# Kernel optimization log

Hardware: AMD Instinct MI355X
Metric: run time of the kernel (lower is better)

Reference implementation:

```python
import jax, jax.numpy as jnp
import numpy as np

N = 65536          # particles
E = 524288         # relations (avg degree 8)
RIG = 4096         # rigid instance = particles [0, RIG); fluid = [RIG, N)
PSTEPS = 2
ATTR, STATE, RELD, NF = 3, 6, 1, 128
DT = 1.0 / 60.0
MEAN_P = np.zeros(3, np.float32); STD_P = np.ones(3, np.float32)
MEAN_V = np.zeros(3, np.float32); STD_V = np.ones(3, np.float32)


def _lin(x, w, b):
    return x @ w.T + b  # torch Linear convention: w is [out, in]


def setup_inputs() -> dict:
    key = jax.random.key(0)
    ks = iter(jax.random.split(key, 40))
    d = {}
    d["state"] = jax.random.normal(next(ks), (N, STATE), jnp.float32)
    d["attr"] = jax.random.normal(next(ks), (N, ATTR), jnp.float32)
    d["Ra"] = jax.random.normal(next(ks), (E, RELD), jnp.float32)
    d["rel_recv"] = jax.random.randint(next(ks), (E,), 0, N, jnp.int32)
    d["rel_send"] = jax.random.randint(next(ks), (E,), 0, N, jnp.int32)

    def w(shape):
        return jax.random.normal(next(ks), shape, jnp.float32) / np.sqrt(shape[1])

    d["pe_w0"] = w((NF, ATTR + 2 * STATE)); d["pe_b0"] = jnp.zeros(NF)
    d["pe_w1"] = w((NF, NF)); d["pe_b1"] = jnp.zeros(NF)
    d["re_w0"] = w((NF, 2 * ATTR + 4 * STATE + RELD)); d["re_b0"] = jnp.zeros(NF)
    d["re_w1"] = w((NF, NF)); d["re_b1"] = jnp.zeros(NF)
    d["re_w2"] = w((NF, NF)); d["re_b2"] = jnp.zeros(NF)
    d["rp_w"] = w((NF, 3 * NF)); d["rp_b"] = jnp.zeros(NF)
    d["pp_w"] = w((NF, 2 * NF)); d["pp_b"] = jnp.zeros(NF)
    d["rg_w0"] = w((NF, NF)); d["rg_b0"] = jnp.zeros(NF)
    d["rg_w1"] = w((NF, NF)); d["rg_b1"] = jnp.zeros(NF)
    d["rg_w2"] = w((7, NF)); d["rg_b2"] = jnp.zeros(7)
    d["fl_w0"] = w((NF, NF)); d["fl_b0"] = jnp.zeros(NF)
    d["fl_w1"] = w((NF, NF)); d["fl_b1"] = jnp.zeros(NF)
    d["fl_w2"] = w((3, NF)); d["fl_b2"] = jnp.zeros(3)
    return d


def reference(state, attr, Ra, rel_recv, rel_send,
              pe_w0, pe_b0, pe_w1, pe_b1,
              re_w0, re_b0, re_w1, re_b1, re_w2, re_b2,
              rp_w, rp_b, pp_w, pp_b,
              rg_w0, rg_b0, rg_w1, rg_b1, rg_w2, rg_b2,
              fl_w0, fl_b0, fl_w1, fl_b1, fl_w2, fl_b2):
    relu = jax.nn.relu
    mean_p = jnp.asarray(MEAN_P); std_p = jnp.asarray(STD_P)
    mean_v = jnp.asarray(MEAN_V); std_v = jnp.asarray(STD_V)

    # rigid-body offset (state minus instance centroid for the rigid instance)
    offset = jnp.zeros_like(state).at[:RIG].set(
        state[:RIG] - jnp.mean(state[:RIG], axis=0))
    attr2 = jnp.concatenate([attr, offset], axis=1)        # [N, ATTR+STATE]

    # f_O^enc: particle encoder on [attr2, state]
    pe_in = jnp.concatenate([attr2, state], axis=1)         # [N, 15]
    particle_encode = relu(_lin(relu(_lin(pe_in, pe_w0, pe_b0)), pe_w1, pe_b1))

    # f_R^enc: relation encoder on gathered receiver/sender features
    rel_in = jnp.concatenate([attr2[rel_recv], attr2[rel_send],
                              state[rel_recv], state[rel_send], Ra], axis=1)  # [E, 31]
    h = relu(_lin(rel_in, re_w0, re_b0))
    h = relu(_lin(h, re_w1, re_b1))
    relation_encode = relu(_lin(h, re_w2, re_b2))           # [E, NF]

    # propagation: gather effects -> f_R -> scatter-add -> f_O
    effect = jnp.zeros((N, NF), state.dtype)
    for _ in range(PSTEPS):
        r_eff = effect[rel_recv]                            # [E, NF]
        s_eff = effect[rel_send]                            # [E, NF]
        rel_eff = relu(_lin(jnp.concatenate(
            [relation_encode, r_eff, s_eff], axis=1), rp_w, rp_b))
        agg = jax.ops.segment_sum(rel_eff, rel_recv, num_segments=N)  # Rr @ rel_eff
        effect = relu(_lin(jnp.concatenate(
            [particle_encode, agg], axis=1), pp_w, pp_b))   # residual=False

    # rigid predictor: quaternion + translation of the rigid body
    pooled = jnp.mean(effect[:RIG], axis=0)                 # [NF]
    t = _lin(relu(_lin(relu(_lin(pooled, rg_w0, rg_b0)), rg_w1, rg_b1)), rg_w2, rg_b2)
    q = t[:4] / jnp.linalg.norm(t[:4])
    w, x, y, z = q[0], q[1], q[2], q[3]
    R = jnp.stack([
        jnp.stack([1.0 - 2 * (y * y + z * z), 2 * (x * y + z * w), 2 * (x * z - y * w)]),
        jnp.stack([2 * (x * y - z * w), 1.0 - 2 * (x * x + z * z), 2 * (y * z + x * w)]),
        jnp.stack([2 * (x * z + y * w), 2 * (y * z - x * w), 1.0 - 2 * (x * x + y * y)]),
    ])
    b = t[4:] * std_p
    p0 = state[:RIG, :3] * std_p + mean_p
    c = jnp.mean(p0, axis=0)
    p1 = (p0 - c) @ R + b + c
    v = (p1 - p0) / DT
    pred_rigid = (v - mean_v) / std_v                       # [RIG, 3]

    # fluid predictor: per-particle MLP
    f = relu(_lin(effect[RIG:], fl_w0, fl_b0))
    f = relu(_lin(f, fl_w1, fl_b1))
    pred_fluid = _lin(f, fl_w2, fl_b2)                      # [N-RIG, 3]

    return jnp.concatenate([pred_rigid, pred_fluid], axis=0)  # [N, 3]
```

## Files before the change

kernel.cpp:

```cpp
#include <hip/hip_runtime.h>
#include <hip/hip_bf16.h>
#include <cstdio>

#define N_P   65536
#define N_E   524288
#define RIG_  4096

typedef __attribute__((ext_vector_type(8))) short bf16x8;
typedef __attribute__((ext_vector_type(4))) float f32x4;
typedef unsigned short u16;
typedef unsigned int   u32;

__device__ __forceinline__ u16 f2b(float x) {
    __hip_bfloat16 h = __float2bfloat16(x);
    return *(u16*)&h;
}
__device__ __forceinline__ float b2f(u16 u) {
    union { unsigned u; float f; } c; c.u = ((unsigned)u) << 16; return c.f;
}
__device__ __forceinline__ unsigned pk2(float x, float y) {
    return (unsigned)f2b(x) | ((unsigned)f2b(y) << 16);
}
#define MFMA(a,b,c) __builtin_amdgcn_mfma_f32_16x16x32_bf16((a),(b),(c),0,0,0)

__device__ __forceinline__ void bar_l() {
    asm volatile("s_waitcnt lgkmcnt(0)\n\ts_barrier" ::: "memory");
}

__global__ __launch_bounds__(256) void k_hist(const int* __restrict__ recv,
                                              u32* __restrict__ cnt) {
    int i = blockIdx.x * 256 + threadIdx.x;
    if (i < N_E) atomicAdd(&cnt[recv[i]], 1u);
}
__global__ __launch_bounds__(256) void k_scan1(u32* __restrict__ data,
                                               u32* __restrict__ bsum) {
    __shared__ u32 s[256];
    int t = threadIdx.x, g = blockIdx.x * 256 + t;
    u32 v = data[g];
    s[t] = v; __syncthreads();
    for (int o = 1; o < 256; o <<= 1) {
        u32 x = (t >= o) ? s[t - o] : 0u;
        __syncthreads(); s[t] += x; __syncthreads();
    }
    data[g] = s[t] - v;
    if (t == 255) bsum[blockIdx.x] = s[255];
}
__global__ __launch_bounds__(256) void k_scan2(u32* __restrict__ bsum) {
    __shared__ u32 s[256];
    int t = threadIdx.x;
    u32 v = bsum[t];
    s[t] = v; __syncthreads();
    for (int o = 1; o < 256; o <<= 1) {
        u32 x = (t >= o) ? s[t - o] : 0u;
        __syncthreads(); s[t] += x; __syncthreads();
    }
    bsum[t] = s[t] - v;
}
__global__ __launch_bounds__(256) void k_scan3(u32* __restrict__ data,
                                               const u32* __restrict__ bsum) {
    int g = blockIdx.x * 256 + threadIdx.x;
    data[g] += bsum[blockIdx.x];
}
__global__ __launch_bounds__(256) void k_scatter(const int* __restrict__ recv,
                                                 const int* __restrict__ send,
                                                 u32* __restrict__ head,
                                                 int4* __restrict__ edges) {
    int i = blockIdx.x * 256 + threadIdx.x;
    if (i < N_E) {
        int n = recv[i];
        u32 pos = atomicAdd(&head[n], 1u);
        edges[pos] = make_int4(n, send[i], i, 0);
    }
}

struct CvtJob { const float* src; u16* dst; int n; int mode; int bstart; };
struct CvtArgs { CvtJob j[14]; };

__global__ __launch_bounds__(256) void k_cvt_all(CvtArgs a) {
    int b = blockIdx.x;
    int ji = 0;
    #pragma unroll
    for (int k = 1; k < 14; k++) if (b >= a.j[k].bstart) ji = k;
    CvtJob jb = a.j[ji];
    int i = (b - jb.bstart) * 256 + threadIdx.x;
    if (i >= jb.n) return;
    if (jb.mode == 0) {
        jb.dst[i] = f2b(jb.src[i]);
    } else if (jb.mode == 2) {
        int r = i >> 7;
        jb.dst[i] = (r < 3) ? f2b(jb.src[i]) : 0;
    } else if (jb.mode == 3) {
        int r = i >> 7, c = i & 127;
        jb.dst[i] = f2b(jb.src[r * 384 + c]);
    } else if (jb.mode == 4) {
        int r = i >> 7, c = i & 127;
        jb.dst[i] = f2b(jb.src[r * 256 + c]);
    } else if (jb.mode == 5) {
        int r = i >> 5, c = i & 31;
        float v = 0.f;
        if (c < 9)       v = jb.src[r * 31 + c];
        else if (c < 15) v = jb.src[r * 31 + 18 + (c - 9)];
        jb.dst[i] = f2b(v);
    } else if (jb.mode == 6) {
        int r = i >> 5, c = i & 31;
        float v = 0.f;
        if (c < 9)       v = jb.src[r * 31 + 9 + c];
        else if (c < 15) v = jb.src[r * 31 + 24 + (c - 9)];
        jb.dst[i] = f2b(v);
    } else {
        int r = i >> 5, c = i & 31;
        jb.dst[i] = (c < 15) ? f2b(jb.src[r * 15 + c]) : 0;
    }
}

__global__ __launch_bounds__(256) void k_centroid(const float* __restrict__ state,
                                                  float* __restrict__ cent) {
    int d = blockIdx.x;
    __shared__ float red[256];
    float s = 0.f;
    for (int r = threadIdx.x; r < RIG_; r += 256) s += state[r * 6 + d];
    red[threadIdx.x] = s; __syncthreads();
    for (int o = 128; o > 0; o >>= 1) {
        if (threadIdx.x < o) red[threadIdx.x] += red[threadIdx.x + o];
        __syncthreads();
    }
    if (threadIdx.x == 0) cent[d] = red[0] / (float)RIG_;
}

__global__ __launch_bounds__(256) void k_particle_ext(
        const float* __restrict__ state, const float* __restrict__ attr,
        const float* __restrict__ cent,
        const u16* __restrict__ w0r, const u16* __restrict__ w0s,
        const u16* __restrict__ pew0, const float* __restrict__ pe_b0,
        const u16* __restrict__ pew1, const float* __restrict__ pe_b1,
        const u16* __restrict__ wp,
        u16* __restrict__ P, u16* __restrict__ Q, u16* __restrict__ T) {
    __shared__ float in_s[64][16];
    __shared__ u16 INF[64 * 32];
    __shared__ __align__(16) u16 BUF[64 * 128];
    __shared__ float b0_s[128], b1_s[128];
    int t = threadIdx.x;
    int base = blockIdx.x * 64;
    if (t < 128) { b0_s[t] = pe_b0[t]; b1_s[t] = pe_b1[t]; }
    for (int it = t; it < 64 * 15; it += 256) {
        int r = it / 15, c = it % 15;
        int p = base + r;
        float v;
        if (c < 3)      v = attr[p * 3 + c];
        else if (c < 9) v = (p < RIG_) ? (state[p * 6 + (c - 3)] - cent[c - 3]) : 0.0f;
        else            v = state[p * 6 + (c - 9)];
        in_s[r][c] = v;
    }
    __syncthreads();
    int wv = t >> 6, kq4 = (t >> 4) & 3, m = t & 15;
    {
        int e = wv * 16 + m;
        u16 tmp[8];
        #pragma unroll
        for (int j = 0; j < 8; j++) {
            int k = kq4 * 8 + j;
            tmp[j] = (k < 15) ? f2b(in_s[e][k]) : (u16)0;
        }
        *(uint4*)&INF[((wv * 4 + kq4) * 16 + m) * 8] = *(uint4*)tmp;
    }
    int lane = t & 63, mm = lane & 15, quad = lane >> 4;
    bf16x8 af0 = *(const bf16x8*)&INF[((wv * 4 + quad) * 16 + mm) * 8];
    {
        f32x4 acc[8] = {};
        #pragma unroll
        for (int nt = 0; nt < 8; nt++) {
            bf16x8 bf = *(const bf16x8*)(w0r + (size_t)(nt * 16 + mm) * 32 + quad * 8);
            acc[nt] = MFMA(af0, bf, acc[nt]);
        }
        #pragma unroll
        for (int nt = 0; nt < 8; nt++) {
            int col = nt * 16 + mm;
            #pragma unroll
            for (int rg = 0; rg < 4; rg++) {
                int row = wv * 16 + quad * 4 + rg;
                P[(size_t)(base + row) * 128 + col] = f2b(acc[nt][rg]);
            }
        }
    }
    {
        f32x4 acc[8] = {};
        #pragma unroll
        for (int nt = 0; nt < 8; nt++) {
            bf16x8 bf = *(const bf16x8*)(w0s + (size_t)(nt * 16 + mm) * 32 + quad * 8);
            acc[nt] = MFMA(af0, bf, acc[nt]);
        }
        #pragma unroll
        for (int nt = 0; nt < 8; nt++) {
            int col = nt * 16 + mm;
            #pragma unroll
            for (int rg = 0; rg < 4; rg++) {
                int row = wv * 16 + quad * 4 + rg;
                Q[(size_t)(base + row) * 128 + col] = f2b(acc[nt][rg]);
            }
        }
    }
    {
        f32x4 acc[8] = {};
        #pragma unroll
        for (int nt = 0; nt < 8; nt++) {
            bf16x8 bf = *(const bf16x8*)(pew0 + (size_t)(nt * 16 + mm) * 32 + quad * 8);
            acc[nt] = MFMA(af0, bf, acc[nt]);
        }
        #pragma unroll
        for (int nt = 0; nt < 8; nt++) {
            int col = nt * 16 + mm;
            #pragma unroll
            for (int rg = 0; rg < 4; rg++) {
                BUF[((wv * 16 + (col >> 3)) * 16 + quad * 4 + rg) * 8 + (col & 7)] =
                    f2b(fmaxf(acc[nt][rg] + b0_s[col], 0.f));
            }
        }
    }
    {
        f32x4 acc[8] = {};
        for (int kc = 0; kc < 4; kc++) {
            bf16x8 af = *(const bf16x8*)&BUF[((wv * 16 + kc * 4 + quad) * 16 + mm) * 8];
            #pragma unroll
            for (int nt = 0; nt < 8; nt++) {
                bf16x8 bf = *(const bf16x8*)(pew1 + (size_t)(nt * 16 + mm) * 128 + kc * 32 + quad * 8);
                acc[nt] = MFMA(af, bf, acc[nt]);
            }
        }
        #pragma unroll
        for (int nt = 0; nt < 8; nt++) {
            int col = nt * 16 + mm;
            #pragma unroll
            for (int rg = 0; rg < 4; rg++) {
                BUF[((wv * 16 + (col >> 3)) * 16 + quad * 4 + rg) * 8 + (col & 7)] =
                    f2b(fmaxf(acc[nt][rg] + b1_s[col], 0.f));
            }
        }
    }
    {
        f32x4 acc[8] = {};
        for (int kc = 0; kc < 4; kc++) {
            bf16x8 af = *(const bf16x8*)&BUF[((wv * 16 + kc * 4 + quad) * 16 + mm) * 8];
            #pragma unroll
            for (int nt = 0; nt < 8; nt++) {
                bf16x8 bf = *(const bf16x8*)(wp + (size_t)(nt * 16 + mm) * 128 + kc * 32 + quad * 8);
                acc[nt] = MFMA(af, bf, acc[nt]);
            }
        }
        #pragma unroll
        for (int nt = 0; nt < 8; nt++) {
            int col = nt * 16 + mm;
            #pragma unroll
            for (int rg = 0; rg < 4; rg++) {
                int row = wv * 16 + quad * 4 + rg;
                T[(size_t)(base + row) * 128 + col] = f2b(acc[nt][rg]);
            }
        }
    }
}

__global__ __launch_bounds__(512, 4) void k_rel(
        const u16* __restrict__ P, const u16* __restrict__ Q,
        const float* __restrict__ Ra, const int4* __restrict__ edges,
        const float* __restrict__ re_w0_raw, const float* __restrict__ b0,
        const u16* __restrict__ w1b, const float* __restrict__ b1,
        const u16* __restrict__ w2b, const float* __restrict__ b2,
        const u16* __restrict__ wreb, const float* __restrict__ rpb,
        u16* __restrict__ Z, float* __restrict__ agg) {
    __shared__ __align__(16) u16 BUFA[64 * 136];
    __shared__ __align__(16) u16 BUFB[64 * 136];
    __shared__ int rv_s[2][64];
    __shared__ float wRa_s[128], b0_s[128], rpb_s[128];
    int t = threadIdx.x;
    if (t < 128) {
        wRa_s[t] = re_w0_raw[t * 31 + 30];
        b0_s[t] = b0[t]; rpb_s[t] = rpb[t];
    }
    int w = t >> 6, lane = t & 63, mm = lane & 15, quad = lane >> 4;
    int colw = w * 16 + mm;
    bf16x8 W1f[4], W2f[4], WEf[4];
    #pragma unroll
    for (int kc = 0; kc < 4; kc++) {
        W1f[kc] = *(const bf16x8*)(w1b  + (size_t)colw * 128 + kc * 32 + quad * 8);
        W2f[kc] = *(const bf16x8*)(w2b  + (size_t)colw * 128 + kc * 32 + quad * 8);
        WEf[kc] = *(const bf16x8*)(wreb + (size_t)colw * 128 + kc * 32 + quad * 8);
    }
    float b1c = b1[colw], b2c = b2[colw];
    int es = t >> 3, cs2 = (t & 7) * 2;
    int egs = es >> 4, ms = es & 15;
    int sseg = t >> 7, cseg = t & 127;
    int zrow = t >> 3, zc0 = (t & 7) * 16;
    const long NT = N_E / 64;
    const long stride = gridDim.x;

    long tile = blockIdx.x;
    uint4 upC0, upC1, uqC0, uqC1; float raC; int rvC;
    {
        long nb = tile * 64;
        int4 e = edges[nb + es];
        rvC = edges[nb + (t & 63)].x;
        raC = Ra[e.z];
        upC0 = *(const uint4*)(P + (size_t)e.x * 128 + (size_t)cs2 * 8);
        upC1 = *(const uint4*)(P + (size_t)e.x * 128 + (size_t)(cs2 + 1) * 8);
        uqC0 = *(const uint4*)(Q + (size_t)e.y * 128 + (size_t)cs2 * 8);
        uqC1 = *(const uint4*)(Q + (size_t)e.y * 128 + (size_t)(cs2 + 1) * 8);
    }
    __syncthreads();
    int p = 0;
    for (; tile < NT; tile += stride) {
        long base = tile * 64;
        long ntile = tile + stride;
        bool hn = ntile < NT;
        int4 eN = make_int4(0, 0, 0, 0); int rvN = 0;
        if (hn) {
            long nb = ntile * 64;
            eN  = edges[nb + es];
            rvN = edges[nb + (t & 63)].x;
        }
        if (t < 64) rv_s[p][t] = rvC;
        {
            #pragma unroll
            for (int ci = 0; ci < 2; ci++) {
                int kq = cs2 + ci;
                uint4 up = ci ? upC1 : upC0;
                uint4 uq = ci ? uqC1 : uqC0;
                const u16* pp = (const u16*)&up; const u16* qq = (const u16*)&uq;
                u16 outv[8];
                #pragma unroll
                for (int j = 0; j < 8; j++) {
                    int c = kq * 8 + j;
                    float v = b2f(pp[j]) + b2f(qq[j]) + raC * wRa_s[c] + b0_s[c];
                    outv[j] = f2b(fmaxf(v, 0.f));
                }
                *(uint4*)&BUFA[((egs * 16 + kq) * 16 + ms) * 8] = *(uint4*)outv;
            }
        }
        bar_l();
        uint4 upN0{}, upN1{}, uqN0{}, uqN1{}; float raN = 0.f;
        if (hn) {
            raN  = Ra[eN.z];
            upN0 = *(const uint4*)(P + (size_t)eN.x * 128 + (size_t)cs2 * 8);
            upN1 = *(const uint4*)(P + (size_t)eN.x * 128 + (size_t)(cs2 + 1) * 8);
            uqN0 = *(const uint4*)(Q + (size_t)eN.y * 128 + (size_t)cs2 * 8);
            uqN1 = *(const uint4*)(Q + (size_t)eN.y * 128 + (size_t)(cs2 + 1) * 8);
        }
        {
            f32x4 acc[4] = {};
            #pragma unroll
            for (int eg = 0; eg < 4; eg++)
                #pragma unroll
                for (int kc = 0; kc < 4; kc++) {
                    bf16x8 af = *(const bf16x8*)&BUFA[((eg * 16 + kc * 4 + quad) * 16 + mm) * 8];
                    acc[eg] = MFMA(af, W1f[kc], acc[eg]);
                }
            #pragma unroll
            for (int eg = 0; eg < 4; eg++)
                #pragma unroll
                for (int rg = 0; rg < 4; rg++)
                    BUFB[((eg * 16 + (colw >> 3)) * 16 + quad * 4 + rg) * 8 + (colw & 7)] =
                        f2b(fmaxf(acc[eg][rg] + b1c, 0.f));
        }
        bar_l();
        {
            f32x4 acc[4] = {};
            #pragma unroll
            for (int eg = 0; eg < 4; eg++)
                #pragma unroll
                for (int kc = 0; kc < 4; kc++) {
                    bf16x8 af = *(const bf16x8*)&BUFB[((eg * 16 + kc * 4 + quad) * 16 + mm) * 8];
                    acc[eg] = MFMA(af, W2f[kc], acc[eg]);
                }
            #pragma unroll
            for (int eg = 0; eg < 4; eg++)
                #pragma unroll
                for (int rg = 0; rg < 4; rg++)
                    BUFA[((eg * 16 + (colw >> 3)) * 16 + quad * 4 + rg) * 8 + (colw & 7)] =
                        f2b(fmaxf(acc[eg][rg] + b2c, 0.f));
        }
        bar_l();
        {
            f32x4 zacc[4] = {};
            #pragma unroll
            for (int eg = 0; eg < 4; eg++)
                #pragma unroll
                for (int kc = 0; kc < 4; kc++) {
                    bf16x8 af = *(const bf16x8*)&BUFA[((eg * 16 + kc * 4 + quad) * 16 + mm) * 8];
                    zacc[eg] = MFMA(af, WEf[kc], zacc[eg]);
                }
            #pragma unroll
            for (int eg = 0; eg < 4; eg++)
                #pragma unroll
                for (int rg = 0; rg < 4; rg++)
                    BUFB[(eg * 16 + quad * 4 + rg) * 136 + colw] = f2b(zacc[eg][rg]);
        }
        bar_l();
        {
            uint4 z0 = *(const uint4*)&BUFB[zrow * 136 + zc0];
            uint4 z1 = *(const uint4*)&BUFB[zrow * 136 + zc0 + 8];
            *(uint4*)&Z[(base + zrow) * 128 + zc0]     = z0;
            *(uint4*)&Z[(base + zrow) * 128 + zc0 + 8] = z1;
        }
        {
            int r0 = sseg * 16;
            int cur = rv_s[p][r0];
            float a = fmaxf(b2f(BUFB[r0 * 136 + cseg]) + rpb_s[cseg], 0.f);
            bool first = true;
            for (int rr = r0 + 1; rr < r0 + 16; rr++) {
                int n = rv_s[p][rr];
                float v = fmaxf(b2f(BUFB[rr * 136 + cseg]) + rpb_s[cseg], 0.f);
                if (n == cur) a += v;
                else {
                    if (first) atomicAdd(&agg[(size_t)cur * 128 + cseg], a);
                    else       agg[(size_t)cur * 128 + cseg] = a;
                    first = false; cur = n; a = v;
                }
            }
            atomicAdd(&agg[(size_t)cur * 128 + cseg], a);
        }
        if (hn) { upC0 = upN0; upC1 = upN1; uqC0 = uqN0; uqC1 = uqN1; raC = raN; rvC = rvN; }
        p ^= 1;
    }
}

__global__ __launch_bounds__(256) void k_node2(
        const float* __restrict__ agg, const u16* __restrict__ T,
        const u16* __restrict__ wab, const float* __restrict__ ppb,
        const u16* __restrict__ wrb, const u16* __restrict__ wsb,
        u16* __restrict__ U, u16* __restrict__ V) {
    __shared__ __align__(16) u16 AF[64 * 128];
    int t = threadIdx.x;
    long base = (long)blockIdx.x * 64;
    int wv = t >> 6, kq4 = (t >> 4) & 3, m = t & 15;
    {
        long node = base + wv * 16 + m;
        #pragma unroll
        for (int i = 0; i < 4; i++) {
            int kq = kq4 + 4 * i;
            const float* src = agg + node * 128 + kq * 8;
            float4 f0 = *(const float4*)src, f1 = *(const float4*)(src + 4);
            uint4 v;
            v.x = pk2(f0.x, f0.y); v.y = pk2(f0.z, f0.w);
            v.z = pk2(f1.x, f1.y); v.w = pk2(f1.z, f1.w);
            *(uint4*)&AF[((wv * 16 + kq) * 16 + m) * 8] = v;
        }
    }
    int lane = t & 63, mm = lane & 15, quad = lane >> 4;
    f32x4 acc[8] = {};
    for (int kc = 0; kc < 4; kc++) {
        bf16x8 af = *(const bf16x8*)&AF[((wv * 16 + kc * 4 + quad) * 16 + mm) * 8];
        #pragma unroll
        for (int nt = 0; nt < 8; nt++) {
            bf16x8 bf = *(const bf16x8*)(wab + (size_t)(nt * 16 + mm) * 128 + kc * 32 + quad * 8);
            acc[nt] = MFMA(af, bf, acc[nt]);
        }
    }
    #pragma unroll
    for (int nt = 0; nt < 8; nt++) {
        int col = nt * 16 + mm;
        #pragma unroll
        for (int rg = 0; rg < 4; rg++) {
            long row = base + wv * 16 + quad * 4 + rg;
            float v = acc[nt][rg] + b2f(T[row * 128 + col]) + ppb[col];
            u16 e = f2b(fmaxf(v, 0.f));
            AF[((wv * 16 + (col >> 3)) * 16 + quad * 4 + rg) * 8 + (col & 7)] = e;
        }
    }
    {
        f32x4 au[8] = {};
        for (int kc = 0; kc < 4; kc++) {
            bf16x8 af = *(const bf16x8*)&AF[((wv * 16 + kc * 4 + quad) * 16 + mm) * 8];
            #pragma unroll
            for (int nt = 0; nt < 8; nt++) {
                bf16x8 bu = *(const bf16x8*)(wrb + (size_t)(nt * 16 + mm) * 128 + kc * 32 + quad * 8);
                au[nt] = MFMA(af, bu, au[nt]);
            }
        }
        #pragma unroll
        for (int nt = 0; nt < 8; nt++) {
            int col = nt * 16 + mm;
            #pragma unroll
            for (int rg = 0; rg < 4; rg++) {
                long row = base + wv * 16 + quad * 4 + rg;
                U[row * 128 + col] = f2b(au[nt][rg]);
            }
        }
    }
    {
        f32x4 av[8] = {};
        for (int kc = 0; kc < 4; kc++) {
            bf16x8 af = *(const bf16x8*)&AF[((wv * 16 + kc * 4 + quad) * 16 + mm) * 8];
            #pragma unroll
            for (int nt = 0; nt < 8; nt++) {
                bf16x8 bv = *(const bf16x8*)(wsb + (size_t)(nt * 16 + mm) * 128 + kc * 32 + quad * 8);
                av[nt] = MFMA(af, bv, av[nt]);
            }
        }
        #pragma unroll
        for (int nt = 0; nt < 8; nt++) {
            int col = nt * 16 + mm;
            #pragma unroll
            for (int rg = 0; rg < 4; rg++) {
                long row = base + wv * 16 + quad * 4 + rg;
                V[row * 128 + col] = f2b(av[nt][rg]);
            }
        }
    }
}

#define HPAD 136
__global__ __launch_bounds__(256) void k_node2fl(
        const float* __restrict__ agg, const u16* __restrict__ T,
        const u16* __restrict__ wab, const float* __restrict__ ppb,
        float* __restrict__ pooledsum,
        const u16* __restrict__ w0b, const float* __restrict__ b0,
        const u16* __restrict__ w1b, const float* __restrict__ b1,
        const u16* __restrict__ w2b, const float* __restrict__ b2,
        float* __restrict__ out) {
    __shared__ __align__(16) u16 H[64 * HPAD];
    int t = threadIdx.x;
    long base = (long)blockIdx.x * 64;
    bool fluid = (base >= RIG_);
    int wv = t >> 6, kq4 = (t >> 4) & 3, m = t & 15;
    {
        long node = base + wv * 16 + m;
        #pragma unroll
        for (int i = 0; i < 4; i++) {
            int kq = kq4 + 4 * i;
            const float* src = agg + node * 128 + kq * 8;
            float4 f0 = *(const float4*)src, f1 = *(const float4*)(src + 4);
            uint4 v;
            v.x = pk2(f0.x, f0.y); v.y = pk2(f0.z, f0.w);
            v.z = pk2(f1.x, f1.y); v.w = pk2(f1.z, f1.w);
            *(uint4*)&H[((wv * 16 + kq) * 16 + m) * 8] = v;
        }
    }
    int lane = t & 63, mm = lane & 15, quad = lane >> 4;
    f32x4 acc[8] = {};
    for (int kc = 0; kc < 4; kc++) {
        bf16x8 af = *(const bf16x8*)&H[((wv * 16 + kc * 4 + quad) * 16 + mm) * 8];
        #pragma unroll
        for (int nt = 0; nt < 8; nt++) {
            bf16x8 bf = *(const bf16x8*)(wab + (size_t)(nt * 16 + mm) * 128 + kc * 32 + quad * 8);
            acc[nt] = MFMA(af, bf, acc[nt]);
        }
    }
    __syncthreads();
    #pragma unroll
    for (int nt = 0; nt < 8; nt++) {
        int col = nt * 16 + mm;
        #pragma unroll
        for (int rg = 0; rg < 4; rg++) {
            long row = base + wv * 16 + quad * 4 + rg;
            float v = acc[nt][rg] + b2f(T[row * 128 + col]) + ppb[col];
            H[(wv * 16 + quad * 4 + rg) * HPAD + col] = f2b(fmaxf(v, 0.f));
        }
    }
    if (!fluid) {
        bar_l();
        int col = t & 127, half = t >> 7;
        float s = 0.f;
        for (int r = half * 32; r < half * 32 + 32; r++)
            s += b2f(H[r * HPAD + col]);
        atomicAdd(&pooledsum[col], s);
        return;
    }
    {
        f32x4 a8[8] = {};
        for (int kc = 0; kc < 4; kc++) {
            bf16x8 af = *(const bf16x8*)&H[(wv * 16 + mm) * HPAD + kc * 32 + quad * 8];
            #pragma unroll
            for (int nt = 0; nt < 8; nt++) {
                bf16x8 bf = *(const bf16x8*)(w0b + (size_t)(nt * 16 + mm) * 128 + kc * 32 + quad * 8);
                a8[nt] = MFMA(af, bf, a8[nt]);
            }
        }
        #pragma unroll
        for (int nt = 0; nt < 8; nt++) {
            int col = nt * 16 + mm;
            float bv = b0[col];
            #pragma unroll
            for (int rg = 0; rg < 4; rg++) {
                int row = wv * 16 + quad * 4 + rg;
                H[row * HPAD + col] = f2b(fmaxf(a8[nt][rg] + bv, 0.f));
            }
        }
    }
    {
        f32x4 a8[8] = {};
        for (int kc = 0; kc < 4; kc++) {
            bf16x8 af = *(const bf16x8*)&H[(wv * 16 + mm) * HPAD + kc * 32 + quad * 8];
            #pragma unroll
            for (int nt = 0; nt < 8; nt++) {
                bf16x8 bf = *(const bf16x8*)(w1b + (size_t)(nt * 16 + mm) * 128 + kc * 32 + quad * 8);
                a8[nt] = MFMA(af, bf, a8[nt]);
            }
        }
        #pragma unroll
        for (int nt = 0; nt < 8; nt++) {
            int col = nt * 16 + mm;
            float bv = b1[col];
            #pragma unroll
            for (int rg = 0; rg < 4; rg++) {
                int row = wv * 16 + quad * 4 + rg;
                H[row * HPAD + col] = f2b(fmaxf(a8[nt][rg] + bv, 0.f));
            }
        }
    }
    {
        f32x4 a1 = {};
        for (int kc = 0; kc < 4; kc++) {
            bf16x8 af = *(const bf16x8*)&H[(wv * 16 + mm) * HPAD + kc * 32 + quad * 8];
            bf16x8 bf = *(const bf16x8*)(w2b + (size_t)mm * 128 + kc * 32 + quad * 8);
            a1 = MFMA(af, bf, a1);
        }
        if (mm < 3) {
            float bv = b2[mm];
            #pragma unroll
            for (int rg = 0; rg < 4; rg++) {
                long row = base + wv * 16 + quad * 4 + rg;
                out[row * 3 + mm] = a1[rg] + bv;
            }
        }
    }
}

__global__ __launch_bounds__(256) void k_edge2(
        const u16* __restrict__ Z, const u16* __restrict__ U, const u16* __restrict__ V,
        const int4* __restrict__ edges,
        const float* __restrict__ rpb, float* __restrict__ agg) {
    __shared__ __align__(16) u16 S16[64 * 136];
    __shared__ int rv_s[64];
    __shared__ float rpb_s[128];
    int t = threadIdx.x;
    long base = (long)blockIdx.x * 64;
    if (t < 64) rv_s[t] = edges[base + t].x;
    if (t < 128) rpb_s[t] = rpb[t];
    int r = t >> 2, q = t & 3;
    int4 er = edges[base + r];
    long zb = (base + r) * 128;
    size_t ub = (size_t)er.x * 128, vb = (size_t)er.y * 128;
    bar_l();
    #pragma unroll
    for (int i = 0; i < 4; i++) {
        int c0 = q * 32 + i * 8;
        uint4 uz = *(const uint4*)(Z + zb + c0);
        uint4 uu = *(const uint4*)(U + ub + c0);
        uint4 uv = *(const uint4*)(V + vb + c0);
        const u16* zz = (const u16*)&uz; const u16* pu = (const u16*)&uu; const u16* pv = (const u16*)&uv;
        u16 o[8];
        #pragma unroll
        for (int j = 0; j < 8; j++)
            o[j] = f2b(fmaxf(b2f(zz[j]) + b2f(pu[j]) + b2f(pv[j]) + rpb_s[c0 + j], 0.f));
        *(uint4*)&S16[r * 136 + c0] = *(uint4*)o;
    }
    bar_l();
    {
        int s = t >> 7, col = t & 127;
        int r0 = s * 32;
        int cur = rv_s[r0];
        float a = b2f(S16[r0 * 136 + col]);
        bool first = true;
        for (int rr = r0 + 1; rr < r0 + 32; rr++) {
            int n = rv_s[rr];
            float v = b2f(S16[rr * 136 + col]);
            if (n == cur) a += v;
            else {
                if (first) atomicAdd(&agg[(size_t)cur * 128 + col], a);
                else       agg[(size_t)cur * 128 + col] = a;
                first = false; cur = n; a = v;
            }
        }
        atomicAdd(&agg[(size_t)cur * 128 + col], a);
    }
}

__global__ __launch_bounds__(128) void k_rigid_head(
        const float* __restrict__ pooledsum,
        const float* __restrict__ w0, const float* __restrict__ b0,
        const float* __restrict__ w1, const float* __restrict__ b1,
        const float* __restrict__ w2, const float* __restrict__ b2,
        float* __restrict__ rig) {
    __shared__ float pl[128], ha[128], hb[128], tv[7];
    int t = threadIdx.x;
    pl[t] = pooledsum[t] * (1.0f / (float)RIG_);
    __syncthreads();
    float a = b0[t];
    for (int k = 0; k < 128; k++) a += w0[t * 128 + k] * pl[k];
    ha[t] = fmaxf(a, 0.f);
    __syncthreads();
    a = b1[t];
    for (int k = 0; k < 128; k++) a += w1[t * 128 + k] * ha[k];
    hb[t] = fmaxf(a, 0.f);
    __syncthreads();
    if (t < 7) {
        float s = b2[t];
        for (int k = 0; k < 128; k++) s += w2[t * 128 + k] * hb[k];
        tv[t] = s;
    }
    __syncthreads();
    if (t == 0) {
        float w = tv[0], x = tv[1], y = tv[2], z = tv[3];
        float n = sqrtf(w * w + x * x + y * y + z * z);
        w /= n; x /= n; y /= n; z /= n;
        rig[0] = 1.f - 2.f * (y * y + z * z); rig[1] = 2.f * (x * y + z * w); rig[2] = 2.f * (x * z - y * w);
        rig[3] = 2.f * (x * y - z * w); rig[4] = 1.f - 2.f * (x * x + z * z); rig[5] = 2.f * (y * z + x * w);
        rig[6] = 2.f * (x * z + y * w); rig[7] = 2.f * (y * z - x * w); rig[8] = 1.f - 2.f * (x * x + y * y);
        rig[9] = tv[4]; rig[10] = tv[5]; rig[11] = tv[6];
    }
}

__global__ __launch_bounds__(256) void k_rigid_out(
        const float* __restrict__ state, const float* __restrict__ cent,
        const float* __restrict__ rig, float* __restrict__ out) {
    int i = blockIdx.x * 256 + threadIdx.x;
    if (i >= RIG_) return;
    float p0[3], d[3];
    #pragma unroll
    for (int k = 0; k < 3; k++) { p0[k] = state[i * 6 + k]; d[k] = p0[k] - cent[k]; }
    #pragma unroll
    for (int j = 0; j < 3; j++) {
        float p1 = rig[0 * 3 + j] * d[0] + rig[1 * 3 + j] * d[1] + rig[2 * 3 + j] * d[2]
                 + rig[9 + j] + cent[j];
        out[i * 3 + j] = (p1 - p0[j]) * 60.0f;
    }
}

extern "C" void kernel_launch(void* const* d_in, const int* in_sizes, int n_in,
                              void* d_out, int out_size, void* d_ws, size_t ws_size,
                              hipStream_t stream) {
    const float* state = (const float*)d_in[0];
    const float* attr  = (const float*)d_in[1];
    const float* Ra    = (const float*)d_in[2];
    const int*   recv  = (const int*)d_in[3];
    const int*   send  = (const int*)d_in[4];
    const float* pe_w0 = (const float*)d_in[5];  const float* pe_b0 = (const float*)d_in[6];
    const float* pe_w1 = (const float*)d_in[7];  const float* pe_b1 = (const float*)d_in[8];
    const float* re_w0 = (const float*)d_in[9];  const float* re_b0 = (const float*)d_in[10];
    const float* re_w1 = (const float*)d_in[11]; const float* re_b1 = (const float*)d_in[12];
    const float* re_w2 = (const float*)d_in[13]; const float* re_b2 = (const float*)d_in[14];
    const float* rp_w  = (const float*)d_in[15]; const float* rp_b  = (const float*)d_in[16];
    const float* pp_w  = (const float*)d_in[17]; const float* pp_b  = (const float*)d_in[18];
    const float* rg_w0 = (const float*)d_in[19]; const float* rg_b0 = (const float*)d_in[20];
    const float* rg_w1 = (const float*)d_in[21]; const float* rg_b1 = (const float*)d_in[22];
    const float* rg_w2 = (const float*)d_in[23]; const float* rg_b2 = (const float*)d_in[24];
    const float* fl_w0 = (const float*)d_in[25]; const float* fl_b0 = (const float*)d_in[26];
    const float* fl_w1 = (const float*)d_in[27]; const float* fl_b1 = (const float*)d_in[28];
    const float* fl_w2 = (const float*)d_in[29]; const float* fl_b2 = (const float*)d_in[30];
    float* out = (float*)d_out;

    char* p = (char*)d_ws;
    auto alloc = [&](size_t bytes) { char* r = p; p += (bytes + 255) / 256 * 256; return r; };
    float* cent    = (float*)alloc(8 * 4);
    float* pooled  = (float*)alloc(128 * 4);
    float* rig     = (float*)alloc(16 * 4);
    u32*   rowhead = (u32*)alloc((size_t)N_P * 4);
    u32*   bsum    = (u32*)alloc(256 * 4);
    int4*  edges   = (int4*)alloc((size_t)N_E * 16);
    float* agg     = (float*)alloc((size_t)N_P * 128 * 4);
    u16*   Z       = (u16*)alloc((size_t)N_E * 128 * 2);
    u16*   T       = (u16*)alloc((size_t)N_P * 128 * 2);
    u16*   P       = (u16*)alloc((size_t)N_P * 128 * 2);
    u16*   Q       = (u16*)alloc((size_t)N_P * 128 * 2);
    u16*   wreb    = (u16*)alloc(128 * 128 * 2);
    u16*   wrb     = (u16*)alloc(128 * 128 * 2);
    u16*   wsb     = (u16*)alloc(128 * 128 * 2);
    u16*   wpb     = (u16*)alloc(128 * 128 * 2);
    u16*   wab     = (u16*)alloc(128 * 128 * 2);
    u16*   rw1b    = (u16*)alloc(128 * 128 * 2);
    u16*   rw2b    = (u16*)alloc(128 * 128 * 2);
    u16*   pew1b   = (u16*)alloc(128 * 128 * 2);
    u16*   flw0b   = (u16*)alloc(128 * 128 * 2);
    u16*   flw1b   = (u16*)alloc(128 * 128 * 2);
    u16*   flw2b   = (u16*)alloc(16 * 128 * 2);
    u16*   w0rb    = (u16*)alloc(128 * 32 * 2);
    u16*   w0sb    = (u16*)alloc(128 * 32 * 2);
    u16*   pew0b   = (u16*)alloc(128 * 32 * 2);
    size_t need = (size_t)(p - (char*)d_ws);
    if (ws_size < need) {
        fprintf(stderr, "kernel_launch: ws_size %zu < needed %zu\n", ws_size, need);
        return;
    }
    u16* U = P; u16* V = Q;

    hipMemsetAsync(rowhead, 0, (size_t)N_P * 4, stream);
    k_hist<<<N_E / 256, 256, 0, stream>>>(recv, rowhead);
    k_scan1<<<N_P / 256, 256, 0, stream>>>(rowhead, bsum);
    k_scan2<<<1, 256, 0, stream>>>(bsum);
    k_scan3<<<N_P / 256, 256, 0, stream>>>(rowhead, bsum);
    k_scatter<<<N_E / 256, 256, 0, stream>>>(recv, send, rowhead, edges);

    CvtArgs ca;
    int bs = 0;
    auto addjob = [&](int idx, const float* s, u16* d, int n, int mode) {
        ca.j[idx] = {s, d, n, mode, bs};
        bs += (n + 255) / 256;
    };
    addjob(0,  rp_w,        wreb,  128 * 128, 3);
    addjob(1,  rp_w + 128,  wrb,   128 * 128, 3);
    addjob(2,  rp_w + 256,  wsb,   128 * 128, 3);
    addjob(3,  pp_w,        wpb,   128 * 128, 4);
    addjob(4,  pp_w + 128,  wab,   128 * 128, 4);
    addjob(5,  re_w1,       rw1b,  128 * 128, 0);
    addjob(6,  re_w2,       rw2b,  128 * 128, 0);
    addjob(7,  pe_w1,       pew1b, 128 * 128, 0);
    addjob(8,  fl_w0,       flw0b, 128 * 128, 0);
    addjob(9,  fl_w1,       flw1b, 128 * 128, 0);
    addjob(10, fl_w2,       flw2b, 16 * 128,  2);
    addjob(11, re_w0,       w0rb,  128 * 32,  5);
    addjob(12, re_w0,       w0sb,  128 * 32,  6);
    addjob(13, pe_w0,       pew0b, 128 * 32,  7);
    k_cvt_all<<<bs, 256, 0, stream>>>(ca);

    k_centroid<<<6, 256, 0, stream>>>(state, cent);
    k_particle_ext<<<N_P / 64, 256, 0, stream>>>(state, attr, cent,
                                                 w0rb, w0sb, pew0b, pe_b0,
                                                 pew1b, pe_b1, wpb, P, Q, T);

    hipMemsetAsync(agg, 0, (size_t)N_P * 128 * 4, stream);
    k_rel<<<512, 512, 0, stream>>>(P, Q, Ra, edges,
                                   re_w0, re_b0, rw1b, re_b1, rw2b, re_b2,
                                   wreb, rp_b, Z, agg);
    k_node2<<<N_P / 64, 256, 0, stream>>>(agg, T, wab, pp_b, wrb, wsb, U, V);

    hipMemsetAsync(agg, 0, (size_t)N_P * 128 * 4, stream);
    hipMemsetAsync(pooled, 0, 128 * 4, stream);
    k_edge2<<<N_E / 64, 256, 0, stream>>>(Z, U, V, edges, rp_b, agg);
    k_node2fl<<<N_P / 64, 256, 0, stream>>>(agg, T, wab, pp_b, pooled,
                                            flw0b, fl_b0, flw1b, fl_b1,
                                            flw2b, fl_b2, out);

    k_rigid_head<<<1, 128, 0, stream>>>(pooled, rg_w0, rg_b0, rg_w1, rg_b1, rg_w2, rg_b2, rig);
    k_rigid_out<<<(RIG_ + 255) / 256, 256, 0, stream>>>(state, cent, rig, out);
}
```

Before: 537.7 us.

## Retile k_rel MLP waves to 2x2 MFMA blocks and drop gather prefetch

Each wave now computes a 32-edge by 32-column tile (2x2 MFMA blocks) instead of 64 edges by 16 columns, so each LDS A-fragment load feeds two MFMAs. Register-resident W1/W2 fragments double per wave, and the third-layer weights are now reloaded from global memory every tile instead of being kept in registers. The software prefetch of the next tile's P/Q gathers is removed; gathers now happen synchronously at the start of each tile. The aim is to cut LDS traffic and register pressure, at the cost of exposing gather latency and adding repeated weight loads.

New measurement: 592.7 us. +10.2%, slower.

```diff
diff --git a/kernel.cpp b/kernel.cpp
--- a/kernel.cpp
+++ b/kernel.cpp
@@ -276,15 +276,22 @@
         b0_s[t] = b0[t]; rpb_s[t] = rpb[t];
     }
     int w = t >> 6, lane = t & 63, mm = lane & 15, quad = lane >> 4;
-    int colw = w * 16 + mm;
-    bf16x8 W1f[4], W2f[4], WEf[4];
+    int eh = w & 1, cq = w >> 1;
+    int e0 = eh * 2;
+    bf16x8 W1f[2][4], W2f[2][4];
+    float b1c[2], b2c[2];
+    int colc[2];
     #pragma unroll
-    for (int kc = 0; kc < 4; kc++) {
-        W1f[kc] = *(const bf16x8*)(w1b  + (size_t)colw * 128 + kc * 32 + quad * 8);
-        W2f[kc] = *(const bf16x8*)(w2b  + (size_t)colw * 128 + kc * 32 + quad * 8);
-        WEf[kc] = *(const bf16x8*)(wreb + (size_t)colw * 128 + kc * 32 + quad * 8);
-    }
-    float b1c = b1[colw], b2c = b2[colw];
+    for (int nt = 0; nt < 2; nt++) {
+        int col = cq * 32 + nt * 16 + mm;
+        colc[nt] = col;
+        #pragma unroll
+        for (int kc = 0; kc < 4; kc++) {
+            W1f[nt][kc] = *(const bf16x8*)(w1b + (size_t)col * 128 + kc * 32 + quad * 8);
+            W2f[nt][kc] = *(const bf16x8*)(w2b + (size_t)col * 128 + kc * 32 + quad * 8);
+        }
+        b1c[nt] = b1[col]; b2c[nt] = b2[col];
+    }
     int es = t >> 3, cs2 = (t & 7) * 2;
     int egs = es >> 4, ms = es & 15;
     int sseg = t >> 7, cseg = t & 127;
@@ -293,16 +300,11 @@
     const long stride = gridDim.x;
 
     long tile = blockIdx.x;
-    uint4 upC0, upC1, uqC0, uqC1; float raC; int rvC;
+    int4 eC; int rvC;
     {
         long nb = tile * 64;
-        int4 e = edges[nb + es];
+        eC = edges[nb + es];
         rvC = edges[nb + (t & 63)].x;
-        raC = Ra[e.z];
-        upC0 = *(const uint4*)(P + (size_t)e.x * 128 + (size_t)cs2 * 8);
-        upC1 = *(const uint4*)(P + (size_t)e.x * 128 + (size_t)(cs2 + 1) * 8);
-        uqC0 = *(const uint4*)(Q + (size_t)e.y * 128 + (size_t)cs2 * 8);
-        uqC1 = *(const uint4*)(Q + (size_t)e.y * 128 + (size_t)(cs2 + 1) * 8);
     }
     __syncthreads();
     int p = 0;
@@ -318,79 +320,92 @@
         }
         if (t < 64) rv_s[p][t] = rvC;
         {
+            float ra = Ra[eC.z];
             #pragma unroll
             for (int ci = 0; ci < 2; ci++) {
                 int kq = cs2 + ci;
-                uint4 up = ci ? upC1 : upC0;
-                uint4 uq = ci ? uqC1 : uqC0;
+                uint4 up = *(const uint4*)(P + (size_t)eC.x * 128 + (size_t)kq * 8);
+                uint4 uq = *(const uint4*)(Q + (size_t)eC.y * 128 + (size_t)kq * 8);
                 const u16* pp = (const u16*)&up; const u16* qq = (const u16*)&uq;
                 u16 outv[8];
                 #pragma unroll
                 for (int j = 0; j < 8; j++) {
                     int c = kq * 8 + j;
-                    float v = b2f(pp[j]) + b2f(qq[j]) + raC * wRa_s[c] + b0_s[c];
+                    float v = b2f(pp[j]) + b2f(qq[j]) + ra * wRa_s[c] + b0_s[c];
                     outv[j] = f2b(fmaxf(v, 0.f));
                 }
                 *(uint4*)&BUFA[((egs * 16 + kq) * 16 + ms) * 8] = *(uint4*)outv;
             }
         }
         bar_l();
-        uint4 upN0{}, upN1{}, uqN0{}, uqN1{}; float raN = 0.f;
-        if (hn) {
-            raN  = Ra[eN.z];
-            upN0 = *(const uint4*)(P + (size_t)eN.x * 128 + (size_t)cs2 * 8);
-            upN1 = *(const uint4*)(P + (size_t)eN.x * 128 + (size_t)(cs2 + 1) * 8);
-            uqN0 = *(const uint4*)(Q + (size_t)eN.y * 128 + (size_t)cs2 * 8);
-            uqN1 = *(const uint4*)(Q + (size_t)eN.y * 128 + (size_t)(cs2 + 1) * 8);
-        }
         {
-            f32x4 acc[4] = {};
-            #pragma unroll
-            for (int eg = 0; eg < 4; eg++)
+            f32x4 acc[2][2] = {};
+            #pragma unroll
+            for (int kc = 0; kc < 4; kc++) {
+                bf16x8 afa = *(const bf16x8*)&BUFA[(((e0 + 0) * 16 + kc * 4 + quad) * 16 + mm) * 8];
+                bf16x8 afb = *(const bf16x8*)&BUFA[(((e0 + 1) * 16 + kc * 4 + quad) * 16 + mm) * 8];
+                acc[0][0] = MFMA(afa, W1f[0][kc], acc[0][0]);
+                acc[0][1] = MFMA(afa, W1f[1][kc], acc[0][1]);
+                acc[1][0] = MFMA(afb, W1f[0][kc], acc[1][0]);
+                acc[1][1] = MFMA(afb, W1f[1][kc], acc[1][1]);
+            }
+            #pragma unroll
+            for (int e = 0; e < 2; e++)
                 #pragma unroll
-                for (int kc = 0; kc < 4; kc++) {
-                    bf16x8 af = *(const bf16x8*)&BUFA[((eg * 16 + kc * 4 + quad) * 16 + mm) * 8];
-                    acc[eg] = MFMA(af, W1f[kc], acc[eg]);
+                for (int nt = 0; nt < 2; nt++) {
+                    int col = colc[nt];
+                    #pragma unroll
+                    for (int rg = 0; rg < 4; rg++)
+                        BUFB[(((e0 + e) * 16 + (col >> 3)) * 16 + quad * 4 + rg) * 8 + (col & 7)] =
+                            f2b(fmaxf(acc[e][nt][rg] + b1c[nt], 0.f));
                 }
-            #pragma unroll
-            for (int eg = 0; eg < 4; eg++)
-                #pragma unroll
-                for (int rg = 0; rg < 4; rg++)
-                    BUFB[((eg * 16 + (colw >> 3)) * 16 + quad * 4 + rg) * 8 + (colw & 7)] =
-                        f2b(fmaxf(acc[eg][rg] + b1c, 0.f));
         }
         bar_l();
         {
-            f32x4 acc[4] = {};
-            #pragma unroll
-            for (int eg = 0; eg < 4; eg++)
+            f32x4 acc[2][2] = {};
+            #pragma unroll
+            for (int kc = 0; kc < 4; kc++) {
+                bf16x8 afa = *(const bf16x8*)&BUFB[(((e0 + 0) * 16 + kc * 4 + quad) * 16 + mm) * 8];
+                bf16x8 afb = *(const bf16x8*)&BUFB[(((e0 + 1) * 16 + kc * 4 + quad) * 16 + mm) * 8];
+                acc[0][0] = MFMA(afa, W2f[0][kc], acc[0][0]);
+                acc[0][1] = MFMA(afa, W2f[1][kc], acc[0][1]);
+                acc[1][0] = MFMA(afb, W2f[0][kc], acc[1][0]);
+                acc[1][1] = MFMA(afb, W2f[1][kc], acc[1][1]);
+            }
+            #pragma unroll
+            for (int e = 0; e < 2; e++)
                 #pragma unroll
-                for (int kc = 0; kc < 4; kc++) {
-                    bf16x8 af = *(const bf16x8*)&BUFB[((eg * 16 + kc * 4 + quad) * 16 + mm) * 8];
-                    acc[eg] = MFMA(af, W2f[kc], acc[eg]);
+                for (int nt = 0; nt < 2; nt++) {
+                    int col = colc[nt];
+                    #pragma unroll
+                    for (int rg = 0; rg < 4; rg++)
+                        BUFA[(((e0 + e) * 16 + (col >> 3)) * 16 + quad * 4 + rg) * 8 + (col & 7)] =
+                            f2b(fmaxf(acc[e][nt][rg] + b2c[nt], 0.f));
                 }
-            #pragma unroll
-            for (int eg = 0; eg < 4; eg++)
-                #pragma unroll
-                for (int rg = 0; rg < 4; rg++)
-                    BUFA[((eg * 16 + (colw >> 3)) * 16 + quad * 4 + rg) * 8 + (colw & 7)] =
-                        f2b(fmaxf(acc[eg][rg] + b2c, 0.f));
         }
         bar_l();
         {
-            f32x4 zacc[4] = {};
-            #pragma unroll
-            for (int eg = 0; eg < 4; eg++)
+            f32x4 zacc[2][2] = {};
+            #pragma unroll
+            for (int kc = 0; kc < 4; kc++) {
+                bf16x8 we0 = *(const bf16x8*)(wreb + (size_t)colc[0] * 128 + kc * 32 + quad * 8);
+                bf16x8 we1 = *(const bf16x8*)(wreb + (size_t)colc[1] * 128 + kc * 32 + quad * 8);
+                bf16x8 afa = *(const bf16x8*)&BUFA[(((e0 + 0) * 16 + kc * 4 + quad) * 16 + mm) * 8];
+                bf16x8 afb = *(const bf16x8*)&BUFA[(((e0 + 1) * 16 + kc * 4 + quad) * 16 + mm) * 8];
+                zacc[0][0] = MFMA(afa, we0, zacc[0][0]);
+                zacc[0][1] = MFMA(afa, we1, zacc[0][1]);
+                zacc[1][0] = MFMA(afb, we0, zacc[1][0]);
+                zacc[1][1] = MFMA(afb, we1, zacc[1][1]);
+            }
+            #pragma unroll
+            for (int e = 0; e < 2; e++)
                 #pragma unroll
-                for (int kc = 0; kc < 4; kc++) {
-                    bf16x8 af = *(const bf16x8*)&BUFA[((eg * 16 + kc * 4 + quad) * 16 + mm) * 8];
-                    zacc[eg] = MFMA(af, WEf[kc], zacc[eg]);
+                for (int nt = 0; nt < 2; nt++) {
+                    int col = colc[nt];
+                    #pragma unroll
+                    for (int rg = 0; rg < 4; rg++)
+                        BUFB[((e0 + e) * 16 + quad * 4 + rg) * 136 + col] = f2b(zacc[e][nt][rg]);
                 }
-            #pragma unroll
-            for (int eg = 0; eg < 4; eg++)
-                #pragma unroll
-                for (int rg = 0; rg < 4; rg++)
-                    BUFB[(eg * 16 + quad * 4 + rg) * 136 + colw] = f2b(zacc[eg][rg]);
         }
         bar_l();
         {
@@ -416,7 +431,7 @@
             }
             atomicAdd(&agg[(size_t)cur * 128 + cseg], a);
         }
-        if (hn) { upC0 = upN0; upC1 = upN1; uqC0 = uqN0; uqC1 = uqN1; raC = raN; rvC = rvN; }
+        eC = eN; rvC = rvN;
         p ^= 1;
     }
 }
```

## Make k_node2 persistent with register-resident weight fragments per wave

Applied to the files above, without the earlier changes.

k_node2 becomes a persistent kernel of 512 blocks with 512 threads each, looping over 64-node tiles. Each wave owns a 16-column slice of the output and loads its weight fragments for the three 128x128 matrices into registers once, instead of re-reading the weights from global memory for every tile. Separate LDS buffers hold the input and hidden activations, and the U and V GEMMs share the same A-fragment reads. The trade-off is more barriers per tile and higher register pressure, and this node-side kernel is a small part of the total time.

After: 513.0 us. 4.6% less time.

```diff
diff --git a/kernel.cpp b/kernel.cpp
--- a/kernel.cpp
+++ b/kernel.cpp
@@ -421,87 +421,79 @@
     }
 }
 
-__global__ __launch_bounds__(256) void k_node2(
+__global__ __launch_bounds__(512, 4) void k_node2(
         const float* __restrict__ agg, const u16* __restrict__ T,
         const u16* __restrict__ wab, const float* __restrict__ ppb,
         const u16* __restrict__ wrb, const u16* __restrict__ wsb,
         u16* __restrict__ U, u16* __restrict__ V) {
-    __shared__ __align__(16) u16 AF[64 * 128];
+    __shared__ __align__(16) u16 BUFA[64 * 128];
+    __shared__ __align__(16) u16 BUFB[64 * 128];
     int t = threadIdx.x;
-    long base = (long)blockIdx.x * 64;
-    int wv = t >> 6, kq4 = (t >> 4) & 3, m = t & 15;
-    {
-        long node = base + wv * 16 + m;
-        #pragma unroll
-        for (int i = 0; i < 4; i++) {
-            int kq = kq4 + 4 * i;
-            const float* src = agg + node * 128 + kq * 8;
+    int w = t >> 6, lane = t & 63, mm = lane & 15, quad = lane >> 4;
+    int colw = w * 16 + mm;
+    bf16x8 WAf[4], WRf[4], WSf[4];
+    #pragma unroll
+    for (int kc = 0; kc < 4; kc++) {
+        WAf[kc] = *(const bf16x8*)(wab + (size_t)colw * 128 + kc * 32 + quad * 8);
+        WRf[kc] = *(const bf16x8*)(wrb + (size_t)colw * 128 + kc * 32 + quad * 8);
+        WSf[kc] = *(const bf16x8*)(wsb + (size_t)colw * 128 + kc * 32 + quad * 8);
+    }
+    float ppbc = ppb[colw];
+    int es = t >> 3, cs2 = (t & 7) * 2;
+    int egs = es >> 4, ms = es & 15;
+    const int NTL = N_P / 64;
+    for (int tile = blockIdx.x; tile < NTL; tile += gridDim.x) {
+        long base = (long)tile * 64;
+        __syncthreads();
+        #pragma unroll
+        for (int ci = 0; ci < 2; ci++) {
+            int kq = cs2 + ci;
+            const float* src = agg + (base + es) * 128 + kq * 8;
             float4 f0 = *(const float4*)src, f1 = *(const float4*)(src + 4);
             uint4 v;
             v.x = pk2(f0.x, f0.y); v.y = pk2(f0.z, f0.w);
             v.z = pk2(f1.x, f1.y); v.w = pk2(f1.z, f1.w);
-            *(uint4*)&AF[((wv * 16 + kq) * 16 + m) * 8] = v;
-        }
-    }
-    int lane = t & 63, mm = lane & 15, quad = lane >> 4;
-    f32x4 acc[8] = {};
-    for (int kc = 0; kc < 4; kc++) {
-        bf16x8 af = *(const bf16x8*)&AF[((wv * 16 + kc * 4 + quad) * 16 + mm) * 8];
-        #pragma unroll
-        for (int nt = 0; nt < 8; nt++) {
-            bf16x8 bf = *(const bf16x8*)(wab + (size_t)(nt * 16 + mm) * 128 + kc * 32 + quad * 8);
-            acc[nt] = MFMA(af, bf, acc[nt]);
-        }
-    }
-    #pragma unroll
-    for (int nt = 0; nt < 8; nt++) {
-        int col = nt * 16 + mm;
-        #pragma unroll
-        for (int rg = 0; rg < 4; rg++) {
-            long row = base + wv * 16 + quad * 4 + rg;
-            float v = acc[nt][rg] + b2f(T[row * 128 + col]) + ppb[col];
-            u16 e = f2b(fmaxf(v, 0.f));
-            AF[((wv * 16 + (col >> 3)) * 16 + quad * 4 + rg) * 8 + (col & 7)] = e;
-        }
-    }
-    {
-        f32x4 au[8] = {};
-        for (int kc = 0; kc < 4; kc++) {
-            bf16x8 af = *(const bf16x8*)&AF[((wv * 16 + kc * 4 + quad) * 16 + mm) * 8];
-            #pragma unroll
-            for (int nt = 0; nt < 8; nt++) {
-                bf16x8 bu = *(const bf16x8*)(wrb + (size_t)(nt * 16 + mm) * 128 + kc * 32 + quad * 8);
-                au[nt] = MFMA(af, bu, au[nt]);
-            }
-        }
-        #pragma unroll
-        for (int nt = 0; nt < 8; nt++) {
-            int col = nt * 16 + mm;
-            #pragma unroll
-            for (int rg = 0; rg < 4; rg++) {
-                long row = base + wv * 16 + quad * 4 + rg;
-                U[row * 128 + col] = f2b(au[nt][rg]);
-            }
-        }
-    }
-    {
-        f32x4 av[8] = {};
-        for (int kc = 0; kc < 4; kc++) {
-            bf16x8 af = *(const bf16x8*)&AF[((wv * 16 + kc * 4 + quad) * 16 + mm) * 8];
-            #pragma unroll
-            for (int nt = 0; nt < 8; nt++) {
-                bf16x8 bv = *(const bf16x8*)(wsb + (size_t)(nt * 16 + mm) * 128 + kc * 32 + quad * 8);
-                av[nt] = MFMA(af, bv, av[nt]);
-            }
-        }
-        #pragma unroll
-        for (int nt = 0; nt < 8; nt++) {
-            int col = nt * 16 + mm;
-            #pragma unroll
-            for (int rg = 0; rg < 4; rg++) {
-                long row = base + wv * 16 + quad * 4 + rg;
-                V[row * 128 + col] = f2b(av[nt][rg]);
-            }
+            *(uint4*)&BUFA[((egs * 16 + kq) * 16 + ms) * 8] = v;
+        }
+        bar_l();
+        {
+            f32x4 acc[4] = {};
+            #pragma unroll
+            for (int eg = 0; eg < 4; eg++)
+                #pragma unroll
+                for (int kc = 0; kc < 4; kc++) {
+                    bf16x8 af = *(const bf16x8*)&BUFA[((eg * 16 + kc * 4 + quad) * 16 + mm) * 8];
+                    acc[eg] = MFMA(af, WAf[kc], acc[eg]);
+                }
+            #pragma unroll
+            for (int eg = 0; eg < 4; eg++)
+                #pragma unroll
+                for (int rg = 0; rg < 4; rg++) {
+                    long row = base + eg * 16 + quad * 4 + rg;
+                    float v = acc[eg][rg] + b2f(T[row * 128 + colw]) + ppbc;
+                    BUFB[((eg * 16 + (colw >> 3)) * 16 + quad * 4 + rg) * 8 + (colw & 7)] =
+                        f2b(fmaxf(v, 0.f));
+                }
+        }
+        bar_l();
+        {
+            f32x4 au[4] = {}, av[4] = {};
+            #pragma unroll
+            for (int eg = 0; eg < 4; eg++)
+                #pragma unroll
+                for (int kc = 0; kc < 4; kc++) {
+                    bf16x8 af = *(const bf16x8*)&BUFB[((eg * 16 + kc * 4 + quad) * 16 + mm) * 8];
+                    au[eg] = MFMA(af, WRf[kc], au[eg]);
+                    av[eg] = MFMA(af, WSf[kc], av[eg]);
+                }
+            #pragma unroll
+            for (int eg = 0; eg < 4; eg++)
+                #pragma unroll
+                for (int rg = 0; rg < 4; rg++) {
+                    long row = base + eg * 16 + quad * 4 + rg;
+                    U[row * 128 + colw] = f2b(au[eg][rg]);
+                    V[row * 128 + colw] = f2b(av[eg][rg]);
+                }
         }
     }
 }
@@ -819,7 +811,7 @@
     k_rel<<<512, 512, 0, stream>>>(P, Q, Ra, edges,
                                    re_w0, re_b0, rw1b, re_b1, rw2b, re_b2,
                                    wreb, rp_b, Z, agg);
-    k_node2<<<N_P / 64, 256, 0, stream>>>(agg, T, wab, pp_b, wrb, wsb, U, V);
+    k_node2<<<512, 512, 0, stream>>>(agg, T, wab, pp_b, wrb, wsb, U, V);
 
     hipMemsetAsync(agg, 0, (size_t)N_P * 128 * 4, stream);
     hipMemsetAsync(pooled, 0, 128 * 4, stream);
```
